# Kernel optimization log

Measured on AMD Instinct MI355X. Metric: run time of the kernel, lower is better.

## Reference

```python
import jax, jax.numpy as jnp
import numpy as np
import math

B, T, D, H = 4, 2048, 1024, 16
DH = D // H


def setup_inputs() -> dict:
    key = jax.random.key(0)
    k1, k2, k3 = jax.random.split(key, 3)
    x = jax.random.normal(k1, (B, T, D), dtype=jnp.float32)
    # causal mask: True = masked (positions j > i)
    attn_mask = jnp.triu(jnp.ones((T, T), dtype=bool), k=1)
    key_padding_mask = jnp.zeros((B, T), dtype=bool)  # no padding
    W_qkv = jax.random.normal(k2, (D, 3 * D), dtype=jnp.float32) / math.sqrt(D)
    W_out = jax.random.normal(k3, (D, D), dtype=jnp.float32) / math.sqrt(D)
    return {"x": x, "W_qkv": W_qkv, "W_out": W_out,
            "attn_mask": attn_mask, "key_padding_mask": key_padding_mask}


def reference(x, W_qkv, W_out, attn_mask, key_padding_mask):
    # qkv projection (bias=False)
    qkv = x @ W_qkv                                   # [B,T,3D]
    q, k, v = jnp.split(qkv, 3, axis=-1)              # each [B,T,D]
    # reshape to heads: [B,H,T,DH]
    q = q.reshape(B, T, H, DH).transpose(0, 2, 1, 3)
    k = k.reshape(B, T, H, DH).transpose(0, 2, 1, 3)
    v = v.reshape(B, T, H, DH).transpose(0, 2, 1, 3)
    scale = 1.0 / math.sqrt(DH)
    scores = jnp.einsum('bhqd,bhkd->bhqk', q, k) * scale   # [B,H,T,T]
    neg_inf = jnp.float32(-jnp.inf)
    scores = jnp.where(attn_mask[None, None, :, :], neg_inf, scores)
    scores = jnp.where(key_padding_mask[:, None, None, :], neg_inf, scores)
    attn = jax.nn.softmax(scores, axis=-1)            # dropout p=0.0 -> identity
    out = jnp.einsum('bhqk,bhkd->bhqd', attn, v)      # [B,H,T,DH]
    out = out.transpose(0, 2, 1, 3).reshape(B, T, D)
    return out @ W_out
```

## Files before the change

### kernel.cpp

```cpp
#include <hip/hip_runtime.h>
#include <hip/hip_bf16.h>

#define Bsz 4
#define T 2048
#define D 1024
#define H 16
#define DH 64

typedef unsigned short u16;
typedef __attribute__((ext_vector_type(8))) __bf16 bf16x8;
typedef __attribute__((ext_vector_type(4))) float f32x4;

__device__ inline u16 f2bf(float f) {
  union { float f; unsigned u; } v; v.f = f;
  unsigned r = (v.u + 0x7FFFu + ((v.u >> 16) & 1u)) >> 16;
  return (u16)r;
}
__device__ inline unsigned pack_bf16(float a, float b) {
  union { float f; unsigned u; } A, B; A.f = a; B.f = b;
  unsigned au = A.u + 0x8000u, bu = B.u + 0x8000u;
  return __builtin_amdgcn_perm(bu, au, 0x07060302);
}

__device__ inline void gll16(const u16* g, u16* l) {
  __builtin_amdgcn_global_load_lds((const __attribute__((address_space(1))) void*)g,
                                   (__attribute__((address_space(3))) void*)l, 16, 0, 0);
}

__global__ __launch_bounds__(256) void convert_f32_bf16(const float* __restrict__ in,
                                                        u16* __restrict__ out, int n4) {
  int i = blockIdx.x * 256 + threadIdx.x;
  if (i < n4) {
    float4 v = reinterpret_cast<const float4*>(in)[i];
    ushort4 o;
    o.x = f2bf(v.x); o.y = f2bf(v.y); o.z = f2bf(v.z); o.w = f2bf(v.w);
    reinterpret_cast<ushort4*>(out)[i] = o;
  }
}

__global__ __launch_bounds__(256) void transpose_f32_bf16(const float* __restrict__ in,
                                                          u16* __restrict__ out, int K, int N) {
  __shared__ float tile[32][33];
  int tx = threadIdx.x & 31, ty = threadIdx.x >> 5;
  int n0 = blockIdx.x * 32, k0 = blockIdx.y * 32;
  #pragma unroll
  for (int i = 0; i < 4; ++i)
    tile[ty + i * 8][tx] = in[(size_t)(k0 + ty + i * 8) * N + n0 + tx];
  __syncthreads();
  #pragma unroll
  for (int i = 0; i < 4; ++i)
    out[(size_t)(n0 + ty + i * 8) * K + k0 + tx] = f2bf(tile[tx][ty + i * 8]);
}

template <int MODE>
__global__ __launch_bounds__(512, 2) void gemm256(const u16* __restrict__ A, const u16* __restrict__ BT,
                                                  float* __restrict__ C,
                                                  u16* __restrict__ Qh, u16* __restrict__ Kh,
                                                  u16* __restrict__ VTh, int M, int N, int K) {
  __shared__ alignas(16) u16 SA[4][8192];
  __shared__ alignas(16) u16 SB[4][8192];
  int tid = threadIdx.x;
  int m0 = blockIdx.y * 256, n0 = blockIdx.x * 256;
  int w = tid >> 6, lane = tid & 63;
  int llo = lane & 15, lhi = lane >> 4;
  int wr = w >> 2, wc = w & 3;
  int swz = ((lhi ^ ((llo >> 1) & 3)) << 3);
  int arow = (wr * 128 + llo) * 32;
  int brow = (wc * 64 + llo) * 32;

  int srcCol = (((tid & 3) ^ ((tid >> 3) & 3)) << 3);
  const u16* gA0 = A + (size_t)(m0 + (tid >> 2)) * K + srcCol;
  const u16* gA1 = gA0 + (size_t)128 * K;
  const u16* gB0 = BT + (size_t)(n0 + (tid >> 2)) * K + srcCol;
  const u16* gB1 = gB0 + (size_t)128 * K;

  f32x4 acc[8][4];
  #pragma unroll
  for (int i = 0; i < 8; ++i)
    #pragma unroll
    for (int j = 0; j < 4; ++j) acc[i][j] = (f32x4){0.f, 0.f, 0.f, 0.f};

  int nt = K >> 5;

  #pragma unroll
  for (int p = 0; p < 3; ++p) {
    gll16(gA0 + p * 32, &SA[p][w * 512]);
    gll16(gA1 + p * 32, &SA[p][4096 + w * 512]);
    gll16(gB0 + p * 32, &SB[p][w * 512]);
    gll16(gB1 + p * 32, &SB[p][4096 + w * 512]);
  }
  asm volatile("s_waitcnt vmcnt(8)" ::: "memory");
  __builtin_amdgcn_s_barrier();

  #pragma unroll 4
  for (int t = 0; t < nt; ++t) {
    int buf = t & 3;
    const u16* sa = SA[buf];
    const u16* sb = SB[buf];

    bf16x8 af[8];
    #pragma unroll
    for (int i = 0; i < 8; ++i)
      af[i] = *reinterpret_cast<const bf16x8*>(&sa[arow + i * 512 + swz]);
    bf16x8 b0 = *reinterpret_cast<const bf16x8*>(&sb[brow + swz]);
    bf16x8 b1 = *reinterpret_cast<const bf16x8*>(&sb[brow + 512 + swz]);
    if (t + 3 < nt) {
      gll16(gA0 + (t + 3) * 32, &SA[(t + 3) & 3][w * 512]);
      gll16(gA1 + (t + 3) * 32, &SA[(t + 3) & 3][4096 + w * 512]);
    }
    __builtin_amdgcn_s_barrier();
    asm volatile("s_waitcnt lgkmcnt(0)" ::: "memory");
    __builtin_amdgcn_s_setprio(1);
    #pragma unroll
    for (int i = 0; i < 8; ++i) {
      acc[i][0] = __builtin_amdgcn_mfma_f32_16x16x32_bf16(af[i], b0, acc[i][0], 0, 0, 0);
      acc[i][1] = __builtin_amdgcn_mfma_f32_16x16x32_bf16(af[i], b1, acc[i][1], 0, 0, 0);
    }
    __builtin_amdgcn_s_setprio(0);
    __builtin_amdgcn_s_barrier();

    bf16x8 b2 = *reinterpret_cast<const bf16x8*>(&sb[brow + 1024 + swz]);
    bf16x8 b3 = *reinterpret_cast<const bf16x8*>(&sb[brow + 1536 + swz]);
    if (t + 3 < nt) {
      gll16(gB0 + (t + 3) * 32, &SB[(t + 3) & 3][w * 512]);
      gll16(gB1 + (t + 3) * 32, &SB[(t + 3) & 3][4096 + w * 512]);
    }
    __builtin_amdgcn_s_barrier();
    asm volatile("s_waitcnt lgkmcnt(0)" ::: "memory");
    __builtin_amdgcn_s_setprio(1);
    #pragma unroll
    for (int i = 0; i < 8; ++i) {
      acc[i][2] = __builtin_amdgcn_mfma_f32_16x16x32_bf16(af[i], b2, acc[i][2], 0, 0, 0);
      acc[i][3] = __builtin_amdgcn_mfma_f32_16x16x32_bf16(af[i], b3, acc[i][3], 0, 0, 0);
    }
    __builtin_amdgcn_s_setprio(0);
    if (t + 3 < nt)      asm volatile("s_waitcnt vmcnt(8)" ::: "memory");
    else if (t + 2 < nt) asm volatile("s_waitcnt vmcnt(4)" ::: "memory");
    else if (t + 1 < nt) asm volatile("s_waitcnt vmcnt(0)" ::: "memory");
    __builtin_amdgcn_s_barrier();
    __builtin_amdgcn_sched_barrier(0);
  }

  if (MODE == 0) {
    #pragma unroll
    for (int i = 0; i < 8; ++i) {
      int ml = m0 + wr * 128 + i * 16 + lhi * 4;
      #pragma unroll
      for (int j = 0; j < 4; ++j) {
        int nl = n0 + wc * 64 + j * 16 + llo;
        #pragma unroll
        for (int r = 0; r < 4; ++r)
          C[(size_t)(ml + r) * N + nl] = acc[i][j][r];
      }
    }
  } else {
    int seg = n0 >> 10;
    #pragma unroll
    for (int i = 0; i < 8; ++i) {
      int mbase = m0 + wr * 128 + i * 16 + lhi * 4;
      int t0 = mbase & (T - 1);
      int b_ = mbase >> 11;
      #pragma unroll
      for (int j = 0; j < 4; ++j) {
        int nl = n0 + wc * 64 + j * 16 + llo;
        int h = (nl >> 6) & 15, d = nl & 63;
        int bh = b_ * H + h;
        if (seg == 0) {
          #pragma unroll
          for (int r = 0; r < 4; ++r)
            Qh[((size_t)bh * T + t0 + r) * DH + d] = f2bf(acc[i][j][r] * 0.125f);
        } else if (seg == 1) {
          #pragma unroll
          for (int r = 0; r < 4; ++r)
            Kh[((size_t)bh * T + t0 + r) * DH + d] = f2bf(acc[i][j][r]);
        } else {
          uint2 p;
          p.x = pack_bf16(acc[i][j][0], acc[i][j][1]);
          p.y = pack_bf16(acc[i][j][2], acc[i][j][3]);
          *reinterpret_cast<uint2*>(&VTh[((size_t)bh * DH + d) * T + t0]) = p;
        }
      }
    }
  }
}

template <int MODE>
__global__ __launch_bounds__(256) void gemm128(const u16* __restrict__ A, const u16* __restrict__ BT,
                                               float* __restrict__ C,
                                               u16* __restrict__ Qh, u16* __restrict__ Kh,
                                               u16* __restrict__ VTh, int M, int N, int K) {
  __shared__ u16 As[128][32];
  __shared__ u16 Bs[128][32];
  int tid = threadIdx.x;
  int m0 = blockIdx.y * 128, n0 = blockIdx.x * 128;
  int w = tid >> 6, lane = tid & 63;
  int llo = lane & 15, lhi = lane >> 4;
  int wm = (w >> 1) * 64, wn = (w & 1) * 64;

  f32x4 acc[4][4];
  #pragma unroll
  for (int i = 0; i < 4; ++i)
    #pragma unroll
    for (int j = 0; j < 4; ++j) acc[i][j] = (f32x4){0.f, 0.f, 0.f, 0.f};

  const u16* gA = A + (size_t)(m0 + w * 32 + (lane >> 2)) * K + (lane & 3) * 8;
  const u16* gB = BT + (size_t)(n0 + w * 32 + (lane >> 2)) * K + (lane & 3) * 8;

  for (int k0 = 0; k0 < K; k0 += 32) {
    gll16(gA + k0, &As[w * 32][0]);
    gll16(gA + (size_t)16 * K + k0, &As[w * 32 + 16][0]);
    gll16(gB + k0, &Bs[w * 32][0]);
    gll16(gB + (size_t)16 * K + k0, &Bs[w * 32 + 16][0]);
    __syncthreads();
    bf16x8 af[4], bfr[4];
    #pragma unroll
    for (int i = 0; i < 4; ++i)
      af[i] = *reinterpret_cast<const bf16x8*>(&As[wm + i * 16 + llo][lhi * 8]);
    #pragma unroll
    for (int j = 0; j < 4; ++j)
      bfr[j] = *reinterpret_cast<const bf16x8*>(&Bs[wn + j * 16 + llo][lhi * 8]);
    #pragma unroll
    for (int i = 0; i < 4; ++i)
      #pragma unroll
      for (int j = 0; j < 4; ++j)
        acc[i][j] = __builtin_amdgcn_mfma_f32_16x16x32_bf16(af[i], bfr[j], acc[i][j], 0, 0, 0);
    __syncthreads();
  }

  if (MODE == 0) {
    #pragma unroll
    for (int i = 0; i < 4; ++i)
      #pragma unroll
      for (int j = 0; j < 4; ++j) {
        int nl = n0 + wn + j * 16 + llo;
        #pragma unroll
        for (int r = 0; r < 4; ++r) {
          int ml = m0 + wm + i * 16 + lhi * 4 + r;
          C[(size_t)ml * N + nl] = acc[i][j][r];
        }
      }
  }
}

__global__ __launch_bounds__(1024, 4) void attn_fwd(const u16* __restrict__ Qh, const u16* __restrict__ Kh,
                                                    const u16* __restrict__ VTh, u16* __restrict__ AO) {
  __shared__ u16 QP[16][16][72];
  __shared__ u16 Ks[64][72];
  __shared__ u16 Vs[64][72];
  int tid = threadIdx.x;
  int qp = blockIdx.x, bh = blockIdx.y;
  int w = tid >> 6, lane = tid & 63;
  int llo = lane & 15, lhi = lane >> 4;

  int qrow_s = tid >> 2, qc = tid & 3;
  int krow_s = tid >> 4, kc = tid & 15;
  const u16* kbase = Kh + ((size_t)bh * T + krow_s) * DH + kc * 4;
  const u16* vbase = VTh + ((size_t)bh * DH + krow_s) * T + kc * 4;
  int b = bh >> 4, h = bh & 15;

  #pragma unroll 1
  for (int half = 0; half < 2; ++half) {
    int qt = half ? (7 - qp) : qp;
    int q0 = qt * 256;

    bf16x8 aq[2];
    {
      const uint4* g = reinterpret_cast<const uint4*>(
          Qh + ((size_t)bh * T + q0 + qrow_s) * DH + qc * 16);
      uint4 a = g[0], bb = g[1];
      uint4* dst = reinterpret_cast<uint4*>(&QP[w][qrow_s & 15][qc * 16]);
      dst[0] = a; dst[1] = bb;
      #pragma unroll
      for (int ks = 0; ks < 2; ++ks)
        aq[ks] = *reinterpret_cast<const bf16x8*>(&QP[w][llo][ks * 32 + lhi * 8]);
    }

    f32x4 o[4];
    #pragma unroll
    for (int i = 0; i < 4; ++i) o[i] = (f32x4){0.f, 0.f, 0.f, 0.f};
    float l_run = 0.f;

    int nj = 4 * qt + 4;
    uint2 ka = *reinterpret_cast<const uint2*>(kbase);
    uint2 va = *reinterpret_cast<const uint2*>(vbase);

    #pragma unroll 1
    for (int j = 0; j < nj; ++j) {
      __syncthreads();
      *reinterpret_cast<uint2*>(&Ks[krow_s][kc * 4]) = ka;
      *reinterpret_cast<uint2*>(&Vs[krow_s][kc * 4]) = va;
      if (j + 1 < nj) {
        ka = *reinterpret_cast<const uint2*>(kbase + (size_t)(j + 1) * 64 * DH);
        va = *reinterpret_cast<const uint2*>(vbase + (j + 1) * 64);
      } else if (half == 0) {
        ka = *reinterpret_cast<const uint2*>(kbase);
        va = *reinterpret_cast<const uint2*>(vbase);
      }
      __syncthreads();

      if (q0 + w * 16 + 15 >= j * 64) {
        f32x4 sc[4];
        #pragma unroll
        for (int kt = 0; kt < 4; ++kt) {
          bf16x8 bk0 = *reinterpret_cast<const bf16x8*>(&Ks[kt * 16 + llo][lhi * 8]);
          bf16x8 bk1 = *reinterpret_cast<const bf16x8*>(&Ks[kt * 16 + llo][32 + lhi * 8]);
          f32x4 z = (f32x4){0.f, 0.f, 0.f, 0.f};
          f32x4 t0 = __builtin_amdgcn_mfma_f32_16x16x32_bf16(bk0, aq[0], z, 0, 0, 0);
          sc[kt] = __builtin_amdgcn_mfma_f32_16x16x32_bf16(bk1, aq[1], t0, 0, 0, 0);
        }

        if (j >= 4 * qt) {
          int qrow_g = q0 + w * 16 + llo;
          #pragma unroll
          for (int kt = 0; kt < 4; ++kt)
            #pragma unroll
            for (int r = 0; r < 4; ++r) {
              int key_g = j * 64 + kt * 16 + lhi * 4 + r;
              if (key_g > qrow_g) sc[kt][r] = -__builtin_inff();
            }
        }

        float s_sum = 0.f;
        #pragma unroll
        for (int kt = 0; kt < 4; ++kt)
          #pragma unroll
          for (int r = 0; r < 4; ++r) {
            float p = __expf(sc[kt][r]);
            sc[kt][r] = p;
            s_sum += p;
          }
        s_sum += __shfl_xor(s_sum, 16);
        s_sum += __shfl_xor(s_sum, 32);
        l_run += s_sum;

        #pragma unroll
        for (int kt = 0; kt < 4; ++kt) {
          uint2 p;
          p.x = pack_bf16(sc[kt][0], sc[kt][1]);
          p.y = pack_bf16(sc[kt][2], sc[kt][3]);
          *reinterpret_cast<uint2*>(&QP[w][llo][kt * 16 + lhi * 4]) = p;
        }

        #pragma unroll
        for (int kk2 = 0; kk2 < 2; ++kk2) {
          bf16x8 pa = *reinterpret_cast<const bf16x8*>(&QP[w][llo][kk2 * 32 + lhi * 8]);
          #pragma unroll
          for (int nt = 0; nt < 4; ++nt) {
            bf16x8 bv = *reinterpret_cast<const bf16x8*>(&Vs[nt * 16 + llo][kk2 * 32 + lhi * 8]);
            o[nt] = __builtin_amdgcn_mfma_f32_16x16x32_bf16(pa, bv, o[nt], 0, 0, 0);
          }
        }
      }
    }

    #pragma unroll
    for (int r = 0; r < 4; ++r) {
      float inv = 1.f / __shfl(l_run, lhi * 4 + r);
      int t = q0 + w * 16 + lhi * 4 + r;
      #pragma unroll
      for (int nt = 0; nt < 4; ++nt)
        AO[((size_t)(b * T + t)) * D + h * 64 + nt * 16 + llo] = f2bf(o[nt][r] * inv);
    }
  }
}

extern "C" void kernel_launch(void* const* d_in, const int* in_sizes, int n_in,
                              void* d_out, int out_size, void* d_ws, size_t ws_size,
                              hipStream_t stream) {
  (void)in_sizes; (void)n_in; (void)out_size;
  const float* x = (const float*)d_in[0];
  const float* Wqkv = (const float*)d_in[1];
  const float* Wout = (const float*)d_in[2];
  float* out = (float*)d_out;

  char* ws = (char*)d_ws;
  size_t off = 0;
  u16* xb = (u16*)(ws + off);    off += (size_t)Bsz * T * D * 2;
  u16* WqkvT = (u16*)(ws + off); off += (size_t)3 * D * D * 2;
  u16* WoutT = (u16*)(ws + off); off += (size_t)D * D * 2;
  u16* Qh = (u16*)(ws + off);    off += (size_t)Bsz * H * T * DH * 2;
  u16* Kh = (u16*)(ws + off);    off += (size_t)Bsz * H * T * DH * 2;
  u16* VTh = (u16*)(ws + off);   off += (size_t)Bsz * H * DH * T * 2;
  u16* AO = xb;
  if (ws_size < off) return;

  int n4 = Bsz * T * D / 4;
  convert_f32_bf16<<<(n4 + 255) / 256, 256, 0, stream>>>(x, xb, n4);
  transpose_f32_bf16<<<dim3(3 * D / 32, D / 32), 256, 0, stream>>>(Wqkv, WqkvT, D, 3 * D);
  transpose_f32_bf16<<<dim3(D / 32, D / 32), 256, 0, stream>>>(Wout, WoutT, D, D);
  gemm256<1><<<dim3(3 * D / 256, Bsz * T / 256), 512, 0, stream>>>(xb, WqkvT, nullptr, Qh, Kh, VTh,
                                                                   Bsz * T, 3 * D, D);
  attn_fwd<<<dim3(4, Bsz * H), 1024, 0, stream>>>(Qh, Kh, VTh, AO);
  gemm128<0><<<dim3(D / 128, Bsz * T / 128), 256, 0, stream>>>(AO, WoutT, out, nullptr, nullptr, nullptr,
                                                               Bsz * T, D, D);
}
```

Measured before the change: 286.2 us.

## Restructure GEMM mainloop to 64-wide K tiles with quarter-tile staged double buffering

Rewrites the 256x256 bf16 GEMM main loop to use K-tiles of 64 in a double buffer instead of 32-wide tiles in a 4-deep ring. Each iteration is split into four MFMA phases over tile quadrants, with loads of the next tile's halves interleaved between them. The change also adds an XOR swizzle suited to the 64-column rows and remaps block indices so that neighbouring blocks are grouped by flat index mod 8, to improve L2 locality. The aim is fewer barriers per unit of K and better overlap of global loads with MFMAs, at the cost of more complex vmcnt bookkeeping and shallower prefetch.

Measured after the change: 277.9 us. -2.9%, faster.

```diff
diff --git a/kernel.cpp b/kernel.cpp
--- a/kernel.cpp
+++ b/kernel.cpp
@@ -57,22 +57,26 @@
                                                   float* __restrict__ C,
                                                   u16* __restrict__ Qh, u16* __restrict__ Kh,
                                                   u16* __restrict__ VTh, int M, int N, int K) {
-  __shared__ alignas(16) u16 SA[4][8192];
-  __shared__ alignas(16) u16 SB[4][8192];
+  __shared__ alignas(16) u16 SA[2][256][64];
+  __shared__ alignas(16) u16 SB[2][256][64];
   int tid = threadIdx.x;
-  int m0 = blockIdx.y * 256, n0 = blockIdx.x * 256;
+
+  int flat = blockIdx.y * gridDim.x + blockIdx.x;
+  int cpx = (int)(gridDim.x * gridDim.y) >> 3;
+  int nf = (flat & 7) * cpx + (flat >> 3);
+  int bx = nf % (int)gridDim.x, by = nf / (int)gridDim.x;
+  int m0 = by * 256, n0 = bx * 256;
+
   int w = tid >> 6, lane = tid & 63;
   int llo = lane & 15, lhi = lane >> 4;
   int wr = w >> 2, wc = w & 3;
-  int swz = ((lhi ^ ((llo >> 1) & 3)) << 3);
-  int arow = (wr * 128 + llo) * 32;
-  int brow = (wc * 64 + llo) * 32;
-
-  int srcCol = (((tid & 3) ^ ((tid >> 3) & 3)) << 3);
-  const u16* gA0 = A + (size_t)(m0 + (tid >> 2)) * K + srcCol;
-  const u16* gA1 = gA0 + (size_t)128 * K;
-  const u16* gB0 = BT + (size_t)(n0 + (tid >> 2)) * K + srcCol;
-  const u16* gB1 = gB0 + (size_t)128 * K;
+
+  int cs0 = ((lhi ^ (llo & 7)) << 3);
+  int cs1 = (((4 + lhi) ^ (llo & 7)) << 3);
+
+  int srcCol = (((lane & 7) ^ ((lane >> 3) & 7)) << 3);
+  const u16* gAl = A + (size_t)(m0 + w * 8 + (lane >> 3)) * K + srcCol;
+  const u16* gBl = BT + (size_t)(n0 + w * 8 + (lane >> 3)) * K + srcCol;
 
   f32x4 acc[8][4];
   #pragma unroll
@@ -80,62 +84,108 @@
     #pragma unroll
     for (int j = 0; j < 4; ++j) acc[i][j] = (f32x4){0.f, 0.f, 0.f, 0.f};
 
-  int nt = K >> 5;
-
-  #pragma unroll
-  for (int p = 0; p < 3; ++p) {
-    gll16(gA0 + p * 32, &SA[p][w * 512]);
-    gll16(gA1 + p * 32, &SA[p][4096 + w * 512]);
-    gll16(gB0 + p * 32, &SB[p][w * 512]);
-    gll16(gB1 + p * 32, &SB[p][4096 + w * 512]);
-  }
-  asm volatile("s_waitcnt vmcnt(8)" ::: "memory");
+  int nt = K >> 6;
+
+  auto stA = [&](int buf, int h, int c, int kt) {
+    gll16(gAl + (h * 128 + c * 64) * K + kt * 64, &SA[buf][h * 128 + c * 64 + w * 8][0]);
+  };
+  auto stB = [&](int buf, int h, int c, int kt) {
+    gll16(gBl + (h * 128 + c * 64) * K + kt * 64, &SB[buf][h * 128 + c * 64 + w * 8][0]);
+  };
+
+  stA(0, 0, 0, 0); stA(0, 0, 1, 0); stA(0, 1, 0, 0); stA(0, 1, 1, 0);
+  stB(0, 0, 0, 0); stB(0, 0, 1, 0); stB(0, 1, 0, 0); stB(0, 1, 1, 0);
+  stB(1, 0, 0, 1); stB(1, 0, 1, 1);
+  stA(1, 0, 0, 1); stA(1, 0, 1, 1);
+  asm volatile("s_waitcnt vmcnt(4)" ::: "memory");
   __builtin_amdgcn_s_barrier();
-
-  #pragma unroll 4
+  __builtin_amdgcn_sched_barrier(0);
+
+  bf16x8 aA[4][2], bB[4][2];
+
+  #pragma unroll 2
   for (int t = 0; t < nt; ++t) {
-    int buf = t & 3;
-    const u16* sa = SA[buf];
-    const u16* sb = SB[buf];
-
-    bf16x8 af[8];
-    #pragma unroll
-    for (int i = 0; i < 8; ++i)
-      af[i] = *reinterpret_cast<const bf16x8*>(&sa[arow + i * 512 + swz]);
-    bf16x8 b0 = *reinterpret_cast<const bf16x8*>(&sb[brow + swz]);
-    bf16x8 b1 = *reinterpret_cast<const bf16x8*>(&sb[brow + 512 + swz]);
-    if (t + 3 < nt) {
-      gll16(gA0 + (t + 3) * 32, &SA[(t + 3) & 3][w * 512]);
-      gll16(gA1 + (t + 3) * 32, &SA[(t + 3) & 3][4096 + w * 512]);
-    }
+    int p = t & 1;
+
+    #pragma unroll
+    for (int i = 0; i < 4; ++i) {
+      aA[i][0] = *reinterpret_cast<const bf16x8*>(&SA[p][wr * 128 + i * 16 + llo][cs0]);
+      aA[i][1] = *reinterpret_cast<const bf16x8*>(&SA[p][wr * 128 + i * 16 + llo][cs1]);
+    }
+    #pragma unroll
+    for (int j = 0; j < 2; ++j) {
+      bB[j][0] = *reinterpret_cast<const bf16x8*>(&SB[p][wc * 64 + j * 16 + llo][cs0]);
+      bB[j][1] = *reinterpret_cast<const bf16x8*>(&SB[p][wc * 64 + j * 16 + llo][cs1]);
+    }
+    if (t + 1 < nt) { stA(1 - p, 1, 0, t + 1); stA(1 - p, 1, 1, t + 1); }
     __builtin_amdgcn_s_barrier();
     asm volatile("s_waitcnt lgkmcnt(0)" ::: "memory");
+    __builtin_amdgcn_sched_barrier(0);
     __builtin_amdgcn_s_setprio(1);
     #pragma unroll
-    for (int i = 0; i < 8; ++i) {
-      acc[i][0] = __builtin_amdgcn_mfma_f32_16x16x32_bf16(af[i], b0, acc[i][0], 0, 0, 0);
-      acc[i][1] = __builtin_amdgcn_mfma_f32_16x16x32_bf16(af[i], b1, acc[i][1], 0, 0, 0);
-    }
+    for (int i = 0; i < 4; ++i)
+      #pragma unroll
+      for (int j = 0; j < 2; ++j) {
+        acc[i][j] = __builtin_amdgcn_mfma_f32_16x16x32_bf16(aA[i][0], bB[j][0], acc[i][j], 0, 0, 0);
+        acc[i][j] = __builtin_amdgcn_mfma_f32_16x16x32_bf16(aA[i][1], bB[j][1], acc[i][j], 0, 0, 0);
+      }
     __builtin_amdgcn_s_setprio(0);
     __builtin_amdgcn_s_barrier();
-
-    bf16x8 b2 = *reinterpret_cast<const bf16x8*>(&sb[brow + 1024 + swz]);
-    bf16x8 b3 = *reinterpret_cast<const bf16x8*>(&sb[brow + 1536 + swz]);
-    if (t + 3 < nt) {
-      gll16(gB0 + (t + 3) * 32, &SB[(t + 3) & 3][w * 512]);
-      gll16(gB1 + (t + 3) * 32, &SB[(t + 3) & 3][4096 + w * 512]);
-    }
+    __builtin_amdgcn_sched_barrier(0);
+
+    #pragma unroll
+    for (int j = 2; j < 4; ++j) {
+      bB[j][0] = *reinterpret_cast<const bf16x8*>(&SB[p][wc * 64 + j * 16 + llo][cs0]);
+      bB[j][1] = *reinterpret_cast<const bf16x8*>(&SB[p][wc * 64 + j * 16 + llo][cs1]);
+    }
+    if (t + 1 < nt) { stB(1 - p, 1, 0, t + 1); stB(1 - p, 1, 1, t + 1); }
     __builtin_amdgcn_s_barrier();
     asm volatile("s_waitcnt lgkmcnt(0)" ::: "memory");
+    __builtin_amdgcn_sched_barrier(0);
     __builtin_amdgcn_s_setprio(1);
     #pragma unroll
-    for (int i = 0; i < 8; ++i) {
-      acc[i][2] = __builtin_amdgcn_mfma_f32_16x16x32_bf16(af[i], b2, acc[i][2], 0, 0, 0);
-      acc[i][3] = __builtin_amdgcn_mfma_f32_16x16x32_bf16(af[i], b3, acc[i][3], 0, 0, 0);
-    }
+    for (int i = 0; i < 4; ++i)
+      #pragma unroll
+      for (int j = 2; j < 4; ++j) {
+        acc[i][j] = __builtin_amdgcn_mfma_f32_16x16x32_bf16(aA[i][0], bB[j][0], acc[i][j], 0, 0, 0);
+        acc[i][j] = __builtin_amdgcn_mfma_f32_16x16x32_bf16(aA[i][1], bB[j][1], acc[i][j], 0, 0, 0);
+      }
     __builtin_amdgcn_s_setprio(0);
-    if (t + 3 < nt)      asm volatile("s_waitcnt vmcnt(8)" ::: "memory");
-    else if (t + 2 < nt) asm volatile("s_waitcnt vmcnt(4)" ::: "memory");
+    __builtin_amdgcn_s_barrier();
+    __builtin_amdgcn_sched_barrier(0);
+
+    #pragma unroll
+    for (int i = 0; i < 4; ++i) {
+      aA[i][0] = *reinterpret_cast<const bf16x8*>(&SA[p][wr * 128 + 64 + i * 16 + llo][cs0]);
+      aA[i][1] = *reinterpret_cast<const bf16x8*>(&SA[p][wr * 128 + 64 + i * 16 + llo][cs1]);
+    }
+    if (t + 2 < nt) { stB(p, 0, 0, t + 2); stB(p, 0, 1, t + 2); }
+    __builtin_amdgcn_s_barrier();
+    asm volatile("s_waitcnt lgkmcnt(0)" ::: "memory");
+    __builtin_amdgcn_sched_barrier(0);
+    __builtin_amdgcn_s_setprio(1);
+    #pragma unroll
+    for (int i = 0; i < 4; ++i)
+      #pragma unroll
+      for (int j = 0; j < 2; ++j) {
+        acc[4 + i][j] = __builtin_amdgcn_mfma_f32_16x16x32_bf16(aA[i][0], bB[j][0], acc[4 + i][j], 0, 0, 0);
+        acc[4 + i][j] = __builtin_amdgcn_mfma_f32_16x16x32_bf16(aA[i][1], bB[j][1], acc[4 + i][j], 0, 0, 0);
+      }
+    __builtin_amdgcn_s_setprio(0);
+    __builtin_amdgcn_s_barrier();
+    __builtin_amdgcn_sched_barrier(0);
+
+    if (t + 2 < nt) { stA(p, 0, 0, t + 2); stA(p, 0, 1, t + 2); }
+    __builtin_amdgcn_s_setprio(1);
+    #pragma unroll
+    for (int i = 0; i < 4; ++i)
+      #pragma unroll
+      for (int j = 2; j < 4; ++j) {
+        acc[4 + i][j] = __builtin_amdgcn_mfma_f32_16x16x32_bf16(aA[i][0], bB[j][0], acc[4 + i][j], 0, 0, 0);
+        acc[4 + i][j] = __builtin_amdgcn_mfma_f32_16x16x32_bf16(aA[i][1], bB[j][1], acc[4 + i][j], 0, 0, 0);
+      }
+    __builtin_amdgcn_s_setprio(0);
+    if (t + 2 < nt)      asm volatile("s_waitcnt vmcnt(4)" ::: "memory");
     else if (t + 1 < nt) asm volatile("s_waitcnt vmcnt(0)" ::: "memory");
     __builtin_amdgcn_s_barrier();
     __builtin_amdgcn_sched_barrier(0);
```
